# Kernel tuning notes

Hardware: AMD Instinct MI355X
Metric: run time of the kernel (lower is better)

## Reference

```python
import jax, jax.numpy as jnp
import numpy as np

N_NODES = 20000
N_EDGES = 640000
FEAT = 128


def setup_inputs() -> dict:
    key = jax.random.key(0)
    k1, k2, k3, k4 = jax.random.split(key, 4)
    x = jax.random.normal(k1, (1, N_NODES, FEAT, 4), dtype=jnp.float32)
    edge_index = jax.random.randint(k2, (2, N_EDGES), 0, N_NODES, dtype=jnp.int64)
    # Linear(in_channels=128, out_channels=128): W [out, in], b [out]
    W = jax.random.normal(k3, (FEAT, FEAT), dtype=jnp.float32) * 0.05
    b = jax.random.normal(k4, (FEAT,), dtype=jnp.float32) * 0.05
    return {"x": x, "edge_index": edge_index, "W": W, "b": b}


def reference(x, edge_index, W, b):
    # x: [B, N, F, T]
    B, N, F, T = x.shape
    # permute -> [B, T, N, F]; Linear over feature dim (out == in == F)
    h = jnp.einsum('bnft,of->btno', x, W) + b          # [B, T, N, F]
    h = h.reshape(B * T, N, F)                          # flatten batch*time
    src = edge_index[0]  # message source (x_j)
    dst = edge_index[1]  # scatter target
    msgs = h[:, src, :]                                 # [B*T, E, F] gather
    # scatter-max per target node (PyG aggr='max'); vmap over batch*time
    agg = jax.vmap(lambda m: jax.ops.segment_max(m, dst, num_segments=N))(msgs)
    # nodes with no incoming edges: segment_max yields -inf -> 0 (PyG fill)
    agg = jnp.where(jnp.isneginf(agg), jnp.zeros_like(agg), agg)
    out = agg.reshape(B, T, N, F).transpose(0, 2, 3, 1)  # [B, N, F, T]
    return out
```

## Files before the change

kernel.cpp:

```cpp
#include <hip/hip_runtime.h>
#include <hip/hip_bf16.h>
#include <stdint.h>

#define N_NODES 20000
#define N_EDGES 640000
#define FEAT 128
#define CAPD 128
#define NPHASE 8
#define CNTSTRIDE 16

typedef __attribute__((ext_vector_type(8))) short bf16x8;
typedef __attribute__((ext_vector_type(4))) float f32x4;

__device__ __forceinline__ unsigned pkbf16(float lo, float hi) {
  __hip_bfloat162 p = __float22bfloat162_rn(make_float2(lo, hi));
  return *reinterpret_cast<unsigned*>(&p);
}

__device__ __forceinline__ unsigned short enc16(float f) {
  unsigned a = __float_as_uint(f);
  unsigned b = (a + 0x7FFFu + ((a >> 16) & 1u)) >> 16;
  unsigned s = (unsigned)((int)a >> 31);
  return (unsigned short)((b ^ 0x8000u) ^ (s & 0x7FFFu));
}

__device__ __forceinline__ float dec16(unsigned e) {
  unsigned b = (e & 0x8000u) ? (e ^ 0x8000u) : (e ^ 0xFFFFu);
  return __uint_as_float(b << 16);
}

__device__ __forceinline__ void pmax(unsigned& a, unsigned v) {
  asm("v_pk_max_u16 %0, %0, %1" : "+v"(a) : "v"(v));
}

#define PMX4(v)                                              \
  do {                                                       \
    pmax(a0, (v).x); pmax(a1, (v).y);                        \
    pmax(a2, (v).z); pmax(a3, (v).w);                        \
  } while (0)

__global__ void init_kernel(const float* __restrict__ W,
                            unsigned short* __restrict__ Wbf,
                            int* __restrict__ cnt) {
  int i = blockIdx.x * 256 + threadIdx.x;
  if (i < N_NODES * CNTSTRIDE) cnt[i] = 0;
  if (i < FEAT * FEAT / 2) {
    float2 w = ((const float2*)W)[i];
    ((unsigned*)Wbf)[i] = pkbf16(w.x, w.y);
  }
}

__global__ __launch_bounds__(512) void gemm_scatter_kernel(
    const float4* __restrict__ x, const unsigned short* __restrict__ Wbf,
    const float* __restrict__ b, uint4* __restrict__ h,
    const int* __restrict__ ei, int* __restrict__ cnt,
    unsigned short* __restrict__ csr) {
  __shared__ __align__(16) unsigned short sm[17408 / 2];
  const int tid = threadIdx.x;
  const int n0 = blockIdx.x * 16;

  const int eid = blockIdx.x * 512 + tid;
  int src = ei[eid];
  int dst = ei[N_EDGES + eid];

  const int e0 = tid, e1 = tid + 512;
  const int na = e0 >> 6, fa = e0 & 63;
  const int nb = e1 >> 6, fb = e1 & 63;
  float4 a0 = x[(size_t)(n0 + na) * 128 + 2 * fa];
  float4 c0 = x[(size_t)(n0 + na) * 128 + 2 * fa + 1];
  float4 a1 = x[(size_t)(n0 + nb) * 128 + 2 * fb];
  float4 c1 = x[(size_t)(n0 + nb) * 128 + 2 * fb + 1];

  int pos = atomicAdd(&cnt[dst * CNTSTRIDE], 1);

  ((unsigned*)sm)[(0 * 16 + na) * 68 + fa] = pkbf16(a0.x, c0.x);
  ((unsigned*)sm)[(1 * 16 + na) * 68 + fa] = pkbf16(a0.y, c0.y);
  ((unsigned*)sm)[(2 * 16 + na) * 68 + fa] = pkbf16(a0.z, c0.z);
  ((unsigned*)sm)[(3 * 16 + na) * 68 + fa] = pkbf16(a0.w, c0.w);
  ((unsigned*)sm)[(0 * 16 + nb) * 68 + fb] = pkbf16(a1.x, c1.x);
  ((unsigned*)sm)[(1 * 16 + nb) * 68 + fb] = pkbf16(a1.y, c1.y);
  ((unsigned*)sm)[(2 * 16 + nb) * 68 + fb] = pkbf16(a1.z, c1.z);
  ((unsigned*)sm)[(3 * 16 + nb) * 68 + fb] = pkbf16(a1.w, c1.w);

  if (pos < CAPD) csr[(size_t)dst * CAPD + pos] = (unsigned short)src;

  __syncthreads();

  const int wv = tid >> 6;
  const int l = tid & 63;
  const int col = l & 15;
  const int quad = l >> 4;

  if (wv < 4) {
    f32x4 acc[8];
#pragma unroll
    for (int os = 0; os < 8; ++os) {
      float bv = b[os * 16 + col];
      acc[os] = (f32x4){bv, bv, bv, bv};
    }

#pragma unroll
    for (int k = 0; k < 4; ++k) {
      bf16x8 af = *(const bf16x8*)&sm[(wv * 16 + col) * 136 + k * 32 + quad * 8];
#pragma unroll
      for (int os = 0; os < 8; ++os) {
        bf16x8 bfv = *(const bf16x8*)&Wbf[(os * 16 + col) * 128 + k * 32 + quad * 8];
        acc[os] = __builtin_amdgcn_mfma_f32_16x16x32_bf16(af, bfv, acc[os], 0, 0, 0);
      }
    }

    __syncthreads();

#pragma unroll
    for (int os = 0; os < 8; ++os) {
#pragma unroll
      for (int r = 0; r < 4; ++r) {
        sm[(quad * 4 + r) * 520 + (os * 16 + col) * 4 + wv] = enc16(acc[os][r]);
      }
    }
  } else {
    __syncthreads();
  }
  __syncthreads();

#pragma unroll
  for (int it = 0; it < 2; ++it) {
    int e = tid + it * 512;
    int n = e >> 6, q = e & 63;
    uint4 v = *(const uint4*)&sm[n * 520 + q * 8];
    h[(size_t)(n0 + n) * 64 + q] = v;
  }
}

__global__ __launch_bounds__(256) void agg_kernel(
    const uint4* __restrict__ h, const int* __restrict__ cnt,
    const unsigned short* __restrict__ csr, float4* __restrict__ out) {
  __shared__ __align__(16) unsigned short sidx[32][136];
  const int bid = blockIdx.x;
  const int p = bid & 7;
  const int grp = bid >> 3;
  const int n0 = grp * 32;
  const int tid = threadIdx.x;

  {
    int r = tid >> 3;
    int q = tid & 7;
    const uint4* srow = (const uint4*)(csr + (size_t)(n0 + r) * CAPD);
    *(uint4*)&sidx[r][q * 8] = srow[q];
    *(uint4*)&sidx[r][(q + 8) * 8] = srow[q + 8];
  }
  __syncthreads();

  const int w = tid >> 6;
  const int lane = tid & 63;
  const int g = lane >> 3;
  const int oq = lane & 7;
  const int n = n0 + w * 8 + g;

  int deg = cnt[n * CNTSTRIDE];
  deg = deg > CAPD ? CAPD : deg;

  const unsigned short* myrow = sidx[w * 8 + g];
  int idx0 = (deg > 0) ? (int)myrow[0] : 0;

  int dmax = deg;
#pragma unroll
  for (int d = 8; d <= 32; d <<= 1) {
    int o = __shfl_xor(dmax, d);
    dmax = o > dmax ? o : dmax;
  }
  dmax = __builtin_amdgcn_readfirstlane(dmax);

  unsigned a0 = 0x007F007Fu, a1 = a0, a2 = a0, a3 = a0;
  const char* hb = (const char*)h;
  const unsigned pb = (((unsigned)p * 8 + oq) << 4);

  for (int jb = 0; jb < dmax; jb += 8) {
    uint4 iv = *(const uint4*)&myrow[jb];
    int e0 = (int)(iv.x & 0xFFFFu), e1 = (int)(iv.x >> 16);
    int e2 = (int)(iv.y & 0xFFFFu), e3 = (int)(iv.y >> 16);
    int e4 = (int)(iv.z & 0xFFFFu), e5 = (int)(iv.z >> 16);
    int e6 = (int)(iv.w & 0xFFFFu), e7 = (int)(iv.w >> 16);
    e0 = (jb + 0 < deg) ? e0 : idx0;
    e1 = (jb + 1 < deg) ? e1 : idx0;
    e2 = (jb + 2 < deg) ? e2 : idx0;
    e3 = (jb + 3 < deg) ? e3 : idx0;
    e4 = (jb + 4 < deg) ? e4 : idx0;
    e5 = (jb + 5 < deg) ? e5 : idx0;
    e6 = (jb + 6 < deg) ? e6 : idx0;
    e7 = (jb + 7 < deg) ? e7 : idx0;
    uint4 v0 = *(const uint4*)(hb + (((unsigned)e0 << 10) + pb));
    uint4 v1 = *(const uint4*)(hb + (((unsigned)e1 << 10) + pb));
    uint4 v2 = *(const uint4*)(hb + (((unsigned)e2 << 10) + pb));
    uint4 v3 = *(const uint4*)(hb + (((unsigned)e3 << 10) + pb));
    uint4 v4 = *(const uint4*)(hb + (((unsigned)e4 << 10) + pb));
    uint4 v5 = *(const uint4*)(hb + (((unsigned)e5 << 10) + pb));
    uint4 v6 = *(const uint4*)(hb + (((unsigned)e6 << 10) + pb));
    uint4 v7 = *(const uint4*)(hb + (((unsigned)e7 << 10) + pb));
    PMX4(v0); PMX4(v1); PMX4(v2); PMX4(v3);
    PMX4(v4); PMX4(v5); PMX4(v6); PMX4(v7);
  }

  float4 o0, o1;
  if (deg == 0) {
    o0 = make_float4(0.f, 0.f, 0.f, 0.f);
    o1 = o0;
  } else {
    o0 = make_float4(dec16(a0 & 0xFFFFu), dec16(a0 >> 16),
                     dec16(a1 & 0xFFFFu), dec16(a1 >> 16));
    o1 = make_float4(dec16(a2 & 0xFFFFu), dec16(a2 >> 16),
                     dec16(a3 & 0xFFFFu), dec16(a3 >> 16));
  }
  out[(size_t)n * 128 + p * 16 + oq * 2] = o0;
  out[(size_t)n * 128 + p * 16 + oq * 2 + 1] = o1;
}

extern "C" void kernel_launch(void* const* d_in, const int* in_sizes, int n_in,
                              void* d_out, int out_size, void* d_ws, size_t ws_size,
                              hipStream_t stream) {
  const float* x = (const float*)d_in[0];
  const int* ei = (const int*)d_in[1];
  const float* W = (const float*)d_in[2];
  const float* b = (const float*)d_in[3];
  float* out = (float*)d_out;

  char* ws = (char*)d_ws;
  uint4* h = (uint4*)ws;
  int* cnt = (int*)(ws + 20480000);
  unsigned short* csr = (unsigned short*)(ws + 21760000);
  unsigned short* Wbf = (unsigned short*)(ws + 26880000);

  init_kernel<<<(N_NODES * CNTSTRIDE + 255) / 256, 256, 0, stream>>>(W, Wbf, cnt);
  gemm_scatter_kernel<<<N_NODES / 16, 512, 0, stream>>>((const float4*)x, Wbf, b, h,
                                                        ei, cnt, csr);
  agg_kernel<<<(N_NODES / 32) * NPHASE, 256, 0, stream>>>(h, cnt, csr, (float4*)out);
}
```

Baseline: 180.6 us.

## Split edge scatter into dedicated blocks and spread GEMM over all eight waves

The fused GEMM+scatter kernel now assigns every third block to CSR scatter only, each handling 1024 edges, while the other blocks do the 16-node GEMM tile. In the GEMM blocks all 8 waves now compute, each covering half of the output columns, where before only 4 waves computed and the rest idled. The aim is to separate atomic-latency-bound scatter work from MFMA work and improve wave utilisation, at the cost of a grid shape of 1875 blocks built from modulo index mapping.

```diff
diff --git a/kernel.cpp b/kernel.cpp
--- a/kernel.cpp
+++ b/kernel.cpp
@@ -57,11 +57,24 @@
     unsigned short* __restrict__ csr) {
   __shared__ __align__(16) unsigned short sm[17408 / 2];
   const int tid = threadIdx.x;
-  const int n0 = blockIdx.x * 16;
-
-  const int eid = blockIdx.x * 512 + tid;
-  int src = ei[eid];
-  int dst = ei[N_EDGES + eid];
+  const int bid = blockIdx.x;
+  const int m3 = bid % 3;
+
+  if (m3 == 2) {
+    const int base = (bid / 3) * 1024;
+#pragma unroll
+    for (int r = 0; r < 2; ++r) {
+      int e = base + r * 512 + tid;
+      int src = ei[e];
+      int dst = ei[N_EDGES + e];
+      int pos = atomicAdd(&cnt[dst * CNTSTRIDE], 1);
+      if (pos < CAPD) csr[(size_t)dst * CAPD + pos] = (unsigned short)src;
+    }
+    return;
+  }
+
+  const int tile = (bid / 3) * 2 + m3;
+  const int n0 = tile * 16;
 
   const int e0 = tid, e1 = tid + 512;
   const int na = e0 >> 6, fa = e0 & 63;
@@ -70,8 +83,6 @@
   float4 c0 = x[(size_t)(n0 + na) * 128 + 2 * fa + 1];
   float4 a1 = x[(size_t)(n0 + nb) * 128 + 2 * fb];
   float4 c1 = x[(size_t)(n0 + nb) * 128 + 2 * fb + 1];
-
-  int pos = atomicAdd(&cnt[dst * CNTSTRIDE], 1);
 
   ((unsigned*)sm)[(0 * 16 + na) * 68 + fa] = pkbf16(a0.x, c0.x);
   ((unsigned*)sm)[(1 * 16 + na) * 68 + fa] = pkbf16(a0.y, c0.y);
@@ -82,44 +93,41 @@
   ((unsigned*)sm)[(2 * 16 + nb) * 68 + fb] = pkbf16(a1.z, c1.z);
   ((unsigned*)sm)[(3 * 16 + nb) * 68 + fb] = pkbf16(a1.w, c1.w);
 
-  if (pos < CAPD) csr[(size_t)dst * CAPD + pos] = (unsigned short)src;
-
   __syncthreads();
 
   const int wv = tid >> 6;
   const int l = tid & 63;
   const int col = l & 15;
   const int quad = l >> 4;
-
-  if (wv < 4) {
-    f32x4 acc[8];
-#pragma unroll
-    for (int os = 0; os < 8; ++os) {
-      float bv = b[os * 16 + col];
-      acc[os] = (f32x4){bv, bv, bv, bv};
+  const int t = wv & 3;
+  const int osh = wv >> 2;
+
+  f32x4 acc[4];
+#pragma unroll
+  for (int os = 0; os < 4; ++os) {
+    float bv = b[(osh * 4 + os) * 16 + col];
+    acc[os] = (f32x4){bv, bv, bv, bv};
+  }
+
+#pragma unroll
+  for (int k = 0; k < 4; ++k) {
+    bf16x8 af = *(const bf16x8*)&sm[(t * 16 + col) * 136 + k * 32 + quad * 8];
+#pragma unroll
+    for (int os = 0; os < 4; ++os) {
+      bf16x8 bfv =
+          *(const bf16x8*)&Wbf[((osh * 4 + os) * 16 + col) * 128 + k * 32 + quad * 8];
+      acc[os] = __builtin_amdgcn_mfma_f32_16x16x32_bf16(af, bfv, acc[os], 0, 0, 0);
     }
-
-#pragma unroll
-    for (int k = 0; k < 4; ++k) {
-      bf16x8 af = *(const bf16x8*)&sm[(wv * 16 + col) * 136 + k * 32 + quad * 8];
-#pragma unroll
-      for (int os = 0; os < 8; ++os) {
-        bf16x8 bfv = *(const bf16x8*)&Wbf[(os * 16 + col) * 128 + k * 32 + quad * 8];
-        acc[os] = __builtin_amdgcn_mfma_f32_16x16x32_bf16(af, bfv, acc[os], 0, 0, 0);
-      }
+  }
+
+  __syncthreads();
+
+#pragma unroll
+  for (int os = 0; os < 4; ++os) {
+#pragma unroll
+    for (int r = 0; r < 4; ++r) {
+      sm[(quad * 4 + r) * 520 + ((osh * 4 + os) * 16 + col) * 4 + t] = enc16(acc[os][r]);
     }
-
-    __syncthreads();
-
-#pragma unroll
-    for (int os = 0; os < 8; ++os) {
-#pragma unroll
-      for (int r = 0; r < 4; ++r) {
-        sm[(quad * 4 + r) * 520 + (os * 16 + col) * 4 + wv] = enc16(acc[os][r]);
-      }
-    }
-  } else {
-    __syncthreads();
   }
   __syncthreads();
 
@@ -231,7 +239,7 @@
   unsigned short* Wbf = (unsigned short*)(ws + 26880000);
 
   init_kernel<<<(N_NODES * CNTSTRIDE + 255) / 256, 256, 0, stream>>>(W, Wbf, cnt);
-  gemm_scatter_kernel<<<N_NODES / 16, 512, 0, stream>>>((const float4*)x, Wbf, b, h,
-                                                        ei, cnt, csr);
+  gemm_scatter_kernel<<<1875, 512, 0, stream>>>((const float4*)x, Wbf, b, h,
+                                                ei, cnt, csr);
   agg_kernel<<<(N_NODES / 32) * NPHASE, 256, 0, stream>>>(h, cnt, csr, (float4*)out);
 }
```

After: 168.2 us. 6.9% less time.
